# Performance work log

Hardware: AMD Instinct MI355X
Metric: run time of the kernel (lower is better)

The kernel has to match this reference:

```python
import jax, jax.numpy as jnp
import numpy as np

D_MODEL = 512
N_HEADS = 8
NEG_INF = -1e9
LN_EPS = 1e-5


def setup_inputs() -> dict:
    key = jax.random.key(0)
    ks = jax.random.split(key, 8)
    B, V, T1, D = 8, 32, 192, D_MODEL
    T = T1 - 1
    x = jax.random.normal(ks[0], (B, V, T1, D), dtype=jnp.float32)
    obs_mask = jax.random.randint(ks[1], (B, V, T), 0, 2, dtype=jnp.int32)
    padding_mask = jax.random.randint(ks[2], (B, T), 0, 2) > 0
    s = 1.0 / np.sqrt(D)
    gamma = jnp.ones((D,), jnp.float32)
    beta = jnp.zeros((D,), jnp.float32)
    W_qkv = jax.random.normal(ks[3], (D, 3 * D), dtype=jnp.float32) * s
    W_proj = jax.random.normal(ks[4], (D, D), dtype=jnp.float32) * s
    b_proj = jnp.zeros((D,), jnp.float32)
    return {"x": x, "obs_mask": obs_mask, "padding_mask": padding_mask,
            "gamma": gamma, "beta": beta, "W_qkv": W_qkv,
            "W_proj": W_proj, "b_proj": b_proj}


def reference(x, obs_mask, padding_mask, gamma, beta, W_qkv, W_proj, b_proj):
    B, V, T1, D = x.shape
    H, dh = N_HEADS, D // N_HEADS
    BV = B * V

    x_flat = x.reshape(BV, T1, D)
    # LayerNorm (eval-mode dropout == identity)
    mu = jnp.mean(x_flat, axis=-1, keepdims=True)
    var = jnp.var(x_flat, axis=-1, keepdims=True)
    x_norm = (x_flat - mu) * jax.lax.rsqrt(var + LN_EPS) * gamma + beta

    qkv = (x_norm @ W_qkv).reshape(BV, T1, 3, H, dh)
    qkv = jnp.transpose(qkv, (2, 0, 3, 1, 4))  # (3, BV, H, T1, dh)
    q, k, v = qkv[0], qkv[1], qkv[2]

    # additive observation bias: mask[i] + mask[j] in {0,1,2}
    obs_ext = jnp.concatenate(
        [jnp.ones((B, V, 1), obs_mask.dtype), obs_mask], axis=2
    ).reshape(BV, T1).astype(jnp.float32)
    attn_bias = obs_ext[:, :, None] + obs_ext[:, None, :]  # (BV, T1, T1)

    # padding mask: True = valid; invalid pairs get -1e9
    pad_ext = jnp.concatenate(
        [jnp.ones((B, 1), bool), padding_mask], axis=1
    )  # (B, T1)
    pad_flat = jnp.broadcast_to(pad_ext[:, None, :], (B, V, T1)).reshape(BV, T1)
    pad_attn = pad_flat[:, :, None] & pad_flat[:, None, :]
    attn_bias = attn_bias + jnp.where(pad_attn, 0.0, NEG_INF)

    scale = 1.0 / jnp.sqrt(jnp.asarray(dh, jnp.float32))
    scores = jnp.einsum("bhqd,bhkd->bhqk", q, k) * scale + attn_bias[:, None]
    attn = jax.nn.softmax(scores, axis=-1)
    out = jnp.einsum("bhqk,bhkd->bhqd", attn, v)  # (BV, H, T1, dh)
    out = jnp.transpose(out, (0, 2, 1, 3)).reshape(BV, T1, D)
    out = out @ W_proj + b_proj
    return (x_flat + out).reshape(B, V, T1, D)
```

## Files before the change

### kernel.cpp

```cpp
#include <hip/hip_runtime.h>

#define DEVI __device__ __forceinline__

typedef __attribute__((ext_vector_type(8))) short short8;
typedef __attribute__((ext_vector_type(4))) float f32x4;

DEVI unsigned short f2bf(float f) {
  unsigned int u = __float_as_uint(f);
  u += 0x7fffu + ((u >> 16) & 1u);
  return (unsigned short)(u >> 16);
}

DEVI void gload16(const void* g, void* l) {
  __builtin_amdgcn_global_load_lds((__attribute__((address_space(1))) void*)g,
                                   (__attribute__((address_space(3))) void*)l, 16, 0, 0);
}

__global__ __launch_bounds__(256) void wprep(
    const float* __restrict__ Wq, const float* __restrict__ Wp,
    unsigned short* __restrict__ Wtq, unsigned short* __restrict__ Wtp) {
  int idx = blockIdx.x * 256 + threadIdx.x;
  int stride = gridDim.x * 256;
  for (int i = idx; i < 1536 * 512; i += stride) {
    int n = i >> 9, k = i & 511;
    Wtq[i] = f2bf(Wq[(size_t)k * 1536 + n]);
  }
  for (int i = idx; i < 512 * 512; i += stride) {
    int n = i >> 9, k = i & 511;
    Wtp[i] = f2bf(Wp[(size_t)k * 512 + n]);
  }
}

__global__ __launch_bounds__(256) void ln_kernel(
    const float* __restrict__ x, const float* __restrict__ gamma,
    const float* __restrict__ beta, unsigned short* __restrict__ xn) {
  int tid = threadIdx.x;
  int w = tid >> 6, l = tid & 63;
  size_t row = (size_t)blockIdx.x * 4 + w;
  const float* xr = x + row * 512 + l * 8;
  float4 v0 = *(const float4*)xr;
  float4 v1 = *(const float4*)(xr + 4);
  float s  = v0.x + v0.y + v0.z + v0.w + v1.x + v1.y + v1.z + v1.w;
  float ss = v0.x*v0.x + v0.y*v0.y + v0.z*v0.z + v0.w*v0.w
           + v1.x*v1.x + v1.y*v1.y + v1.z*v1.z + v1.w*v1.w;
  #pragma unroll
  for (int m = 1; m < 64; m <<= 1) {
    s  += __shfl_xor(s,  m);
    ss += __shfl_xor(ss, m);
  }
  float mean = s * (1.f / 512.f);
  float var  = ss * (1.f / 512.f) - mean * mean;
  float rstd = rsqrtf(var + 1e-5f);
  float4 g0 = *(const float4*)(gamma + l * 8);
  float4 g1 = *(const float4*)(gamma + l * 8 + 4);
  float4 b0 = *(const float4*)(beta + l * 8);
  float4 b1 = *(const float4*)(beta + l * 8 + 4);
  short8 ov;
  ov[0] = (short)f2bf((v0.x - mean) * rstd * g0.x + b0.x);
  ov[1] = (short)f2bf((v0.y - mean) * rstd * g0.y + b0.y);
  ov[2] = (short)f2bf((v0.z - mean) * rstd * g0.z + b0.z);
  ov[3] = (short)f2bf((v0.w - mean) * rstd * g0.w + b0.w);
  ov[4] = (short)f2bf((v1.x - mean) * rstd * g1.x + b1.x);
  ov[5] = (short)f2bf((v1.y - mean) * rstd * g1.y + b1.y);
  ov[6] = (short)f2bf((v1.z - mean) * rstd * g1.z + b1.z);
  ov[7] = (short)f2bf((v1.w - mean) * rstd * g1.w + b1.w);
  *(short8*)(xn + row * 512 + l * 8) = ov;
}

template<int EPI>
__global__ __launch_bounds__(256, 2) void gemm_bt(
    const unsigned short* __restrict__ A, const unsigned short* __restrict__ Bt,
    unsigned short* __restrict__ Cbf, float* __restrict__ Cf,
    const float* __restrict__ bias, const float* __restrict__ resid,
    int M, int N, int K, int nbx) {
  __shared__ unsigned short As[128 * 64];
  __shared__ unsigned short Bs[128 * 64];
  int tid = threadIdx.x;
  int w = tid >> 6, l = tid & 63;
  int nwg = nbx * gridDim.y;
  int lin = blockIdx.y * nbx + blockIdx.x;
  int cpx = nwg >> 3;
  int swz = (lin & 7) * cpx + (lin >> 3);
  int bn = swz % nbx, bm = swz / nbx;
  int wr = w >> 1, wc = w & 1;
  int t8 = tid >> 3;
  int c8s = (((tid & 7) ^ ((tid >> 3) & 7)) * 8);
  int lr = l & 15, lk4 = l >> 4;
  const unsigned short* Ab = A + (size_t)bm * 128 * K;
  const unsigned short* Bb = Bt + (size_t)bn * 128 * K;
  f32x4 zero = {0.f, 0.f, 0.f, 0.f};
  f32x4 acc[4][4];
  #pragma unroll
  for (int i = 0; i < 4; i++)
    #pragma unroll
    for (int j = 0; j < 4; j++) acc[i][j] = zero;

  for (int k0 = 0; k0 < K; k0 += 64) {
    #pragma unroll
    for (int i = 0; i < 4; i++) {
      gload16(Ab + (size_t)(i * 32 + t8) * K + k0 + c8s, (char*)As + i * 4096 + w * 1024);
      gload16(Bb + (size_t)(i * 32 + t8) * K + k0 + c8s, (char*)Bs + i * 4096 + w * 1024);
    }
    __syncthreads();
    #pragma unroll
    for (int kk = 0; kk < 2; kk++) {
      short8 a[4], b[4];
      #pragma unroll
      for (int i = 0; i < 4; i++) {
        int ra = wr * 64 + i * 16 + lr;
        a[i] = *(const short8*)((const char*)As + ra * 128 +
                                (((kk * 64 + lk4 * 16)) ^ ((ra & 7) << 4)));
      }
      #pragma unroll
      for (int j = 0; j < 4; j++) {
        int rb = wc * 64 + j * 16 + lr;
        b[j] = *(const short8*)((const char*)Bs + rb * 128 +
                                (((kk * 64 + lk4 * 16)) ^ ((rb & 7) << 4)));
      }
      #pragma unroll
      for (int i = 0; i < 4; i++)
        #pragma unroll
        for (int j = 0; j < 4; j++)
          acc[i][j] = __builtin_amdgcn_mfma_f32_16x16x32_bf16(a[i], b[j], acc[i][j], 0, 0, 0);
    }
    __syncthreads();
  }
  int rb = bm * 128 + wr * 64 + lk4 * 4;
  int cb = bn * 128 + wc * 64 + lr;
  if (EPI == 0) {
    #pragma unroll
    for (int i = 0; i < 4; i++)
      #pragma unroll
      for (int j = 0; j < 4; j++)
        #pragma unroll
        for (int r = 0; r < 4; r++)
          Cbf[(size_t)(rb + i * 16 + r) * N + (cb + j * 16)] = f2bf(acc[i][j][r]);
  } else {
    #pragma unroll
    for (int i = 0; i < 4; i++)
      #pragma unroll
      for (int j = 0; j < 4; j++)
        #pragma unroll
        for (int r = 0; r < 4; r++) {
          int row = rb + i * 16 + r, col = cb + j * 16;
          Cf[(size_t)row * N + col] = acc[i][j][r] + bias[col] + resid[(size_t)row * N + col];
        }
  }
}

__global__ __launch_bounds__(256, 2) void attn_kernel(
    const unsigned short* __restrict__ qkv, unsigned short* __restrict__ aout,
    const int* __restrict__ obs_mask, const int* __restrict__ pad_mask) {
  const int LDV = 200, LDP = 104;
  __shared__ __align__(16) char smem[67072];
  char* KsB = smem;
  unsigned short* Vt = (unsigned short*)smem;
  unsigned short* Pw = (unsigned short*)(smem + 25600);
  float* obsb = (float*)(smem + 65536);
  int*   padb = (int*)(smem + 66304);

  int h = blockIdx.x, bv = blockIdx.y;
  int tid = threadIdx.x, w = tid >> 6, l = tid & 63;
  int lr = l & 15, lk4 = l >> 4;
  int b = bv >> 5;
  for (int t = tid; t < 192; t += 256) {
    obsb[t] = (t == 0) ? 1.f : (float)obs_mask[bv * 191 + (t - 1)];
    padb[t] = (t == 0) ? 1 : pad_mask[b * 191 + (t - 1)];
  }
  const unsigned short* base = qkv + (size_t)bv * 192 * 1536 + h * 64;

  #pragma unroll
  for (int it = 0; it < 6; it++) {
    int s = it * 256 + tid;
    int row = s >> 3, slot = s & 7;
    gload16(base + (size_t)row * 1536 + 512 + (slot ^ (row & 7)) * 8,
            KsB + it * 4096 + w * 1024);
  }
  short8 qf[3][2];
  #pragma unroll
  for (int i = 0; i < 3; i++)
    #pragma unroll
    for (int kk = 0; kk < 2; kk++)
      qf[i][kk] = *(const short8*)(base + (size_t)(w * 48 + i * 16 + lr) * 1536 + kk * 32 + lk4 * 8);

  __syncthreads();
  f32x4 zero = {0.f, 0.f, 0.f, 0.f};
  f32x4 sc[3][12];
  #pragma unroll
  for (int i = 0; i < 3; i++)
    #pragma unroll
    for (int j = 0; j < 12; j++) sc[i][j] = zero;
  #pragma unroll
  for (int kk = 0; kk < 2; kk++) {
    short8 bb[12];
    #pragma unroll
    for (int j = 0; j < 12; j++) {
      int row = j * 16 + lr;
      bb[j] = *(const short8*)(KsB + row * 128 + ((kk * 64 + lk4 * 16) ^ ((row & 7) << 4)));
    }
    #pragma unroll
    for (int i = 0; i < 3; i++)
      #pragma unroll
      for (int j = 0; j < 12; j++)
        sc[i][j] = __builtin_amdgcn_mfma_f32_16x16x32_bf16(qf[i][kk], bb[j], sc[i][j], 0, 0, 0);
  }
  __syncthreads();

  for (int s = tid; s < 192 * 8; s += 256) {
    int row = s >> 3, d0 = (s & 7) * 8;
    short8 vv = *(const short8*)(base + (size_t)row * 1536 + 1024 + d0);
    int slot = ((d0 >> 3) & 7) << 4;
    #pragma unroll
    for (int e = 0; e < 8; e++) {
      int byte = (((d0 + e) * (LDV * 2) + row * 2) ^ slot);
      *(unsigned short*)((char*)Vt + byte) = (unsigned short)vv[e];
    }
  }
  float colobs[12];
  int colpad[12];
  #pragma unroll
  for (int j = 0; j < 12; j++) {
    colobs[j] = obsb[j * 16 + lr];
    colpad[j] = padb[j * 16 + lr];
  }
  #pragma unroll
  for (int i = 0; i < 3; i++) {
    #pragma unroll
    for (int r = 0; r < 4; r++) {
      int row = w * 48 + i * 16 + lk4 * 4 + r;
      float ro = obsb[row];
      int rp = padb[row];
      float vals[12];
      float mx = -3.0e38f;
      #pragma unroll
      for (int j = 0; j < 12; j++) {
        float vv = sc[i][j][r] * 0.125f + ro + colobs[j]
                 + ((rp & colpad[j]) ? 0.f : -1e9f);
        vals[j] = vv;
        mx = fmaxf(mx, vv);
      }
      #pragma unroll
      for (int m = 1; m < 16; m <<= 1) mx = fmaxf(mx, __shfl_xor(mx, m));
      float sum = 0.f;
      #pragma unroll
      for (int j = 0; j < 12; j++) {
        float e = __expf(vals[j] - mx);
        vals[j] = e;
        sum += e;
      }
      #pragma unroll
      for (int m = 1; m < 16; m <<= 1) sum += __shfl_xor(sum, m);
      float inv = 1.f / sum;
      #pragma unroll
      for (int j = 0; j < 12; j++) sc[i][j][r] = vals[j] * inv;
    }
  }
  __syncthreads();

  unsigned short* Pme = Pw + w * 48 * LDP;
  f32x4 o[3][4];
  #pragma unroll
  for (int i = 0; i < 3; i++)
    #pragma unroll
    for (int jd = 0; jd < 4; jd++) o[i][jd] = zero;
  #pragma unroll
  for (int kc = 0; kc < 2; kc++) {
    #pragma unroll
    for (int i = 0; i < 3; i++)
      #pragma unroll
      for (int r = 0; r < 4; r++) {
        int row = i * 16 + lk4 * 4 + r;
        #pragma unroll
        for (int jj = 0; jj < 6; jj++)
          Pme[row * LDP + jj * 16 + lr] = f2bf(sc[i][kc * 6 + jj][r]);
      }
    asm volatile("s_waitcnt lgkmcnt(0)" ::: "memory");
    __builtin_amdgcn_sched_barrier(0);
    #pragma unroll
    for (int kk = 0; kk < 3; kk++) {
      short8 a[3], bb[4];
      #pragma unroll
      for (int i = 0; i < 3; i++)
        a[i] = *(const short8*)&Pme[(i * 16 + lr) * LDP + kk * 32 + lk4 * 8];
      #pragma unroll
      for (int jd = 0; jd < 4; jd++) {
        int d = jd * 16 + lr;
        int byte = ((d * (LDV * 2) + (kc * 96 + kk * 32 + lk4 * 8) * 2) ^ (((d >> 3) & 7) << 4));
        bb[jd] = *(const short8*)((const char*)Vt + byte);
      }
      #pragma unroll
      for (int i = 0; i < 3; i++)
        #pragma unroll
        for (int jd = 0; jd < 4; jd++)
          o[i][jd] = __builtin_amdgcn_mfma_f32_16x16x32_bf16(a[i], bb[jd], o[i][jd], 0, 0, 0);
    }
  }
  unsigned short* ob = aout + (size_t)bv * 192 * 512 + h * 64;
  #pragma unroll
  for (int i = 0; i < 3; i++)
    #pragma unroll
    for (int jd = 0; jd < 4; jd++)
      #pragma unroll
      for (int r = 0; r < 4; r++) {
        int t = w * 48 + i * 16 + lk4 * 4 + r;
        int d = jd * 16 + lr;
        ob[(size_t)t * 512 + d] = f2bf(o[i][jd][r]);
      }
}

extern "C" void kernel_launch(void* const* d_in, const int* in_sizes, int n_in,
                              void* d_out, int out_size, void* d_ws, size_t ws_size,
                              hipStream_t stream) {
  const float* x     = (const float*)d_in[0];
  const int*   obs   = (const int*)d_in[1];
  const int*   pad   = (const int*)d_in[2];
  const float* gamma = (const float*)d_in[3];
  const float* beta  = (const float*)d_in[4];
  const float* Wq    = (const float*)d_in[5];
  const float* Wp    = (const float*)d_in[6];
  const float* bp    = (const float*)d_in[7];
  float* out = (float*)d_out;
  char* ws = (char*)d_ws;

  const size_t M = 49152;
  unsigned short* xn  = (unsigned short*)ws;
  unsigned short* qkv = (unsigned short*)(ws + M * 512 * 2);
  unsigned short* Wtq = (unsigned short*)(ws + M * 512 * 2 + M * 1536 * 2);
  unsigned short* Wtp = Wtq + 1536 * 512;

  wprep<<<dim3(512), dim3(256), 0, stream>>>(Wq, Wp, Wtq, Wtp);
  ln_kernel<<<dim3(12288), dim3(256), 0, stream>>>(x, gamma, beta, xn);
  gemm_bt<0><<<dim3(12, 384), dim3(256), 0, stream>>>(
      xn, Wtq, qkv, nullptr, nullptr, nullptr, 49152, 1536, 512, 12);
  attn_kernel<<<dim3(8, 256), dim3(256), 0, stream>>>(qkv, xn, obs, pad);
  gemm_bt<1><<<dim3(4, 384), dim3(256), 0, stream>>>(
      xn, Wtp, nullptr, out, bp, x, 49152, 512, 512, 4);
}
```

Baseline: 252.7 us.

## Shrink attention LDS footprint for 3 blocks/CU, pack P/V stores, add setprio

The attention kernel's P staging buffer is shrunk from two 96-column chunks to three 64-column chunks with an XOR-swizzled 128-byte row layout. This cuts shared memory from about 67KB to about 52KB so launch bounds can request 3 blocks per CU. The V transpose now writes two keys at a time as 32-bit stores, probabilities are pre-packed to bf16 pairs in registers, and MFMA sections are wrapped in s_setprio. The pf array adds register pressure, which could cause spills at the higher occupancy target, and there is one extra LDS write/wait round per block.

```diff
diff --git a/kernel.cpp b/kernel.cpp
--- a/kernel.cpp
+++ b/kernel.cpp
@@ -9,6 +9,10 @@
   unsigned int u = __float_as_uint(f);
   u += 0x7fffu + ((u >> 16) & 1u);
   return (unsigned short)(u >> 16);
+}
+
+DEVI unsigned int pk2(float lo, float hi) {
+  return ((unsigned int)f2bf(hi) << 16) | (unsigned int)f2bf(lo);
 }
 
 DEVI void gload16(const void* g, void* l) {
@@ -148,16 +152,15 @@
   }
 }
 
-__global__ __launch_bounds__(256, 2) void attn_kernel(
+__global__ __launch_bounds__(256, 3) void attn_kernel(
     const unsigned short* __restrict__ qkv, unsigned short* __restrict__ aout,
     const int* __restrict__ obs_mask, const int* __restrict__ pad_mask) {
-  const int LDV = 200, LDP = 104;
-  __shared__ __align__(16) char smem[67072];
+  __shared__ __align__(16) char smem[51712];
   char* KsB = smem;
   unsigned short* Vt = (unsigned short*)smem;
-  unsigned short* Pw = (unsigned short*)(smem + 25600);
-  float* obsb = (float*)(smem + 65536);
-  int*   padb = (int*)(smem + 66304);
+  char* Pw = smem + 25600;
+  float* obsb = (float*)(smem + 50176);
+  int*   padb = (int*)(smem + 50944);
 
   int h = blockIdx.x, bv = blockIdx.y;
   int tid = threadIdx.x, w = tid >> 6, l = tid & 63;
@@ -198,24 +201,32 @@
       int row = j * 16 + lr;
       bb[j] = *(const short8*)(KsB + row * 128 + ((kk * 64 + lk4 * 16) ^ ((row & 7) << 4)));
     }
+    __builtin_amdgcn_s_setprio(1);
     #pragma unroll
     for (int i = 0; i < 3; i++)
       #pragma unroll
       for (int j = 0; j < 12; j++)
         sc[i][j] = __builtin_amdgcn_mfma_f32_16x16x32_bf16(qf[i][kk], bb[j], sc[i][j], 0, 0, 0);
+    __builtin_amdgcn_s_setprio(0);
   }
   __syncthreads();
 
-  for (int s = tid; s < 192 * 8; s += 256) {
-    int row = s >> 3, d0 = (s & 7) * 8;
-    short8 vv = *(const short8*)(base + (size_t)row * 1536 + 1024 + d0);
+  #pragma unroll
+  for (int it = 0; it < 3; it++) {
+    int s = it * 256 + tid;
+    int kp = s >> 3;
+    int d0 = (s & 7) * 8;
+    short8 va = *(const short8*)(base + (size_t)(kp * 2) * 1536 + 1024 + d0);
+    short8 vb = *(const short8*)(base + (size_t)(kp * 2 + 1) * 1536 + 1024 + d0);
     int slot = ((d0 >> 3) & 7) << 4;
     #pragma unroll
     for (int e = 0; e < 8; e++) {
-      int byte = (((d0 + e) * (LDV * 2) + row * 2) ^ slot);
-      *(unsigned short*)((char*)Vt + byte) = (unsigned short)vv[e];
-    }
-  }
+      int byte = (((d0 + e) * 400 + kp * 4) ^ slot);
+      *(unsigned int*)((char*)Vt + byte) =
+          ((unsigned int)(unsigned short)vb[e] << 16) | (unsigned int)(unsigned short)va[e];
+    }
+  }
+
   float colobs[12];
   int colpad[12];
   #pragma unroll
@@ -223,6 +234,7 @@
     colobs[j] = obsb[j * 16 + lr];
     colpad[j] = padb[j * 16 + lr];
   }
+  unsigned int pf[3][2][12];
   #pragma unroll
   for (int i = 0; i < 3; i++) {
     #pragma unroll
@@ -254,45 +266,59 @@
       #pragma unroll
       for (int j = 0; j < 12; j++) sc[i][j][r] = vals[j] * inv;
     }
+    #pragma unroll
+    for (int j = 0; j < 12; j++) {
+      pf[i][0][j] = pk2(sc[i][j][0], sc[i][j][1]);
+      pf[i][1][j] = pk2(sc[i][j][2], sc[i][j][3]);
+    }
   }
   __syncthreads();
 
-  unsigned short* Pme = Pw + w * 48 * LDP;
+  char* Pme = Pw + w * 6144;
   f32x4 o[3][4];
   #pragma unroll
   for (int i = 0; i < 3; i++)
     #pragma unroll
     for (int jd = 0; jd < 4; jd++) o[i][jd] = zero;
   #pragma unroll
-  for (int kc = 0; kc < 2; kc++) {
+  for (int kc = 0; kc < 3; kc++) {
     #pragma unroll
     for (int i = 0; i < 3; i++)
       #pragma unroll
-      for (int r = 0; r < 4; r++) {
-        int row = i * 16 + lk4 * 4 + r;
-        #pragma unroll
-        for (int jj = 0; jj < 6; jj++)
-          Pme[row * LDP + jj * 16 + lr] = f2bf(sc[i][kc * 6 + jj][r]);
+      for (int rp = 0; rp < 2; rp++) {
+        int row0 = i * 16 + lk4 * 4 + rp * 2;
+        int row1 = row0 + 1;
+        #pragma unroll
+        for (int jj = 0; jj < 4; jj++) {
+          unsigned int v = pf[i][rp][kc * 4 + jj];
+          int c2 = (jj * 16 + lr) * 2;
+          *(unsigned short*)(Pme + row0 * 128 + (c2 ^ ((row0 & 7) << 4))) = (unsigned short)v;
+          *(unsigned short*)(Pme + row1 * 128 + (c2 ^ ((row1 & 7) << 4))) = (unsigned short)(v >> 16);
+        }
       }
     asm volatile("s_waitcnt lgkmcnt(0)" ::: "memory");
     __builtin_amdgcn_sched_barrier(0);
     #pragma unroll
-    for (int kk = 0; kk < 3; kk++) {
+    for (int kk = 0; kk < 2; kk++) {
       short8 a[3], bb[4];
       #pragma unroll
-      for (int i = 0; i < 3; i++)
-        a[i] = *(const short8*)&Pme[(i * 16 + lr) * LDP + kk * 32 + lk4 * 8];
+      for (int i = 0; i < 3; i++) {
+        int ra = i * 16 + lr;
+        a[i] = *(const short8*)(Pme + ra * 128 + (((kk * 32 + lk4 * 8) * 2) ^ ((ra & 7) << 4)));
+      }
       #pragma unroll
       for (int jd = 0; jd < 4; jd++) {
         int d = jd * 16 + lr;
-        int byte = ((d * (LDV * 2) + (kc * 96 + kk * 32 + lk4 * 8) * 2) ^ (((d >> 3) & 7) << 4));
+        int byte = ((d * 400 + (kc * 64 + kk * 32 + lk4 * 8) * 2) ^ (((d >> 3) & 7) << 4));
         bb[jd] = *(const short8*)((const char*)Vt + byte);
       }
+      __builtin_amdgcn_s_setprio(1);
       #pragma unroll
       for (int i = 0; i < 3; i++)
         #pragma unroll
         for (int jd = 0; jd < 4; jd++)
           o[i][jd] = __builtin_amdgcn_mfma_f32_16x16x32_bf16(a[i], bb[jd], o[i][jd], 0, 0, 0);
+      __builtin_amdgcn_s_setprio(0);
     }
   }
   unsigned short* ob = aout + (size_t)bv * 192 * 512 + h * 64;
```

Result: slower. 425.4 us (+68.3%).
